# Kernel tuning notes

Hardware: AMD Instinct MI355X
Metric: run time of the kernel (lower is better)

Reference implementation:

```python
import jax, jax.numpy as jnp
import numpy as np

N_HEADS = 8
FACTOR = 5


def layer_norm(x, g, b, eps=1e-5):
    m = x.mean(-1, keepdims=True)
    v = ((x - m) ** 2).mean(-1, keepdims=True)
    return (x - m) / jnp.sqrt(v + eps) * g + b


def prob_attn(q, k, v, factor, key):
    # q,k,v: [B,H,L,E]; mask_flag=False path of ProbAttention
    B, H, L, E = q.shape
    U = min(int(factor * np.ceil(np.log(L))), L)  # sample_k == n_top (L_Q == L_K)
    idx = jax.random.randint(key, (L, U), 0, L)   # random KV sample per query pos
    k_samp = k[:, :, idx, :]                      # gather: [B,H,L,U,E]
    qk_samp = jnp.einsum('bhle,bhlue->bhlu', q, k_samp)
    M = qk_samp.max(-1) - qk_samp.sum(-1) / L     # sparsity measure [B,H,L]
    _, top = jax.lax.top_k(M, U)                  # top-u query indices [B,H,U]
    q_red = jnp.take_along_axis(q, top[..., None], axis=2)  # [B,H,U,E]
    scores = jnp.einsum('bhue,bhke->bhuk', q_red, k) * (1.0 / np.sqrt(E))
    attn = jax.nn.softmax(scores, axis=-1)
    upd = jnp.einsum('bhuk,bhkd->bhud', attn, v)  # [B,H,U,D]
    ctx = jnp.broadcast_to(v.mean(axis=2, keepdims=True), (B, H, L, v.shape[-1]))
    bi = jnp.arange(B)[:, None, None]
    hi = jnp.arange(H)[None, :, None]
    return ctx.at[bi, hi, top].set(upd)          # scatter reduced context


def informer_fwd(x_enc, x_mark_enc, conv_w, Wq, bq, Wk, bk, Wv, bv, Wo, bo,
                 W1, b1, W2, b2, g1, be1, g2, be2, gF, bF, fc_w, fc_b):
    B, L, C = x_enc.shape
    D = conv_w.shape[0]
    H = N_HEADS
    dh = D // H
    # TokenEmbedding: circular Conv1d k=3, no bias
    xp = jnp.transpose(x_enc, (0, 2, 1))                      # [B,C,L]
    xp = jnp.concatenate([xp[..., -1:], xp, xp[..., :1]], axis=-1)
    tok = jax.lax.conv_general_dilated(xp, conv_w, (1,), 'VALID',
                                       dimension_numbers=('NCH', 'OIH', 'NCH'))
    tok = jnp.transpose(tok, (0, 2, 1))                       # [B,L,D]
    # PositionalEmbedding (sinusoid)
    pos = jnp.arange(L, dtype=jnp.float32)[:, None]
    div = jnp.exp(jnp.arange(0, D, 2, dtype=jnp.float32) * (-np.log(10000.0) / D))
    pe = jnp.zeros((L, D), jnp.float32)
    pe = pe.at[:, 0::2].set(jnp.sin(pos * div)).at[:, 1::2].set(jnp.cos(pos * div))
    x = tok + pe
    n_layers = Wq.shape[0]
    for l in range(n_layers):
        q = (x @ Wq[l].T + bq[l]).reshape(B, L, H, dh).transpose(0, 2, 1, 3)
        k = (x @ Wk[l].T + bk[l]).reshape(B, L, H, dh).transpose(0, 2, 1, 3)
        v = (x @ Wv[l].T + bv[l]).reshape(B, L, H, dh).transpose(0, 2, 1, 3)
        ctx = prob_attn(q, k, v, FACTOR, jax.random.fold_in(jax.random.key(42), l))
        # NOTE: original code does .view(B, L, -1) on [B,H,L,dh] WITHOUT transposing
        out = ctx.reshape(B, L, H * dh)
        x = x + (out @ Wo[l].T + bo[l])
        x = layer_norm(x, g1[l], be1[l])
        y = jax.nn.relu(x @ W1[l].T + b1[l]) @ W2[l].T + b2[l]   # 1x1 convs == dense
        x = layer_norm(x + y, g2[l], be2[l])
    x = layer_norm(x, gF, bF)
    out = x * x_mark_enc[..., None]
    out = out.reshape(B, -1)
    return out @ fc_w.T + fc_b


def setup_inputs() -> dict:
    B, L, C, D, H, Dff, EL, NC = 8, 1024, 32, 512, 8, 2048, 3, 16
    key = jax.random.key(0)
    ks = jax.random.split(key, 16)
    rn = lambda k, s, sc=0.02: sc * jax.random.normal(k, s, dtype=jnp.float32)
    return {
        'x_enc': jax.random.normal(ks[0], (B, L, C), dtype=jnp.float32),
        'x_mark_enc': jax.random.uniform(ks[1], (B, L), dtype=jnp.float32),
        'conv_w': rn(ks[2], (D, C, 3), 0.1),
        'Wq': rn(ks[3], (EL, D, D)), 'bq': jnp.zeros((EL, D)),
        'Wk': rn(ks[4], (EL, D, D)), 'bk': jnp.zeros((EL, D)),
        'Wv': rn(ks[5], (EL, D, D)), 'bv': jnp.zeros((EL, D)),
        'Wo': rn(ks[6], (EL, D, D)), 'bo': jnp.zeros((EL, D)),
        'W1': rn(ks[7], (EL, Dff, D)), 'b1': jnp.zeros((EL, Dff)),
        'W2': rn(ks[8], (EL, D, Dff)), 'b2': jnp.zeros((EL, D)),
        'g1': jnp.ones((EL, D)), 'be1': jnp.zeros((EL, D)),
        'g2': jnp.ones((EL, D)), 'be2': jnp.zeros((EL, D)),
        'gF': jnp.ones((D,)), 'bF': jnp.zeros((D,)),
        'fc_w': rn(ks[9], (NC, L * D)), 'fc_b': jnp.zeros((NC,)),
    }


def reference(x_enc, x_mark_enc, conv_w, Wq, bq, Wk, bk, Wv, bv, Wo, bo,
              W1, b1, W2, b2, g1, be1, g2, be2, gF, bF, fc_w, fc_b):
    return informer_fwd(x_enc, x_mark_enc, conv_w, Wq, bq, Wk, bk, Wv, bv, Wo, bo,
                        W1, b1, W2, b2, g1, be1, g2, be2, gF, bF, fc_w, fc_b)
```

## Files before the change

kernel.cpp:

```cpp
#include <hip/hip_runtime.h>
#include <stdint.h>
#include <math.h>

#define LSEQ   1024
#define DMODEL 512
#define NH     8
#define DH     64
#define DFF    2048
#define NB     8
#define NLAYER 3
#define UTOP   35
#define NCLS   16
#define WPERL  3145728

typedef unsigned short u16;
typedef _Float16 f16x8 __attribute__((ext_vector_type(8)));
typedef __attribute__((ext_vector_type(4))) float f32x4;

__device__ __forceinline__ u16 f2h(float f) {
  _Float16 h = (_Float16)f;
  return __builtin_bit_cast(u16, h);
}
__device__ __forceinline__ float h2f(u16 b) {
  return (float)__builtin_bit_cast(_Float16, b);
}

#define GLDS16(gsrc, ldst)                                                        \
  __builtin_amdgcn_global_load_lds(                                              \
      (const __attribute__((address_space(1))) void*)(gsrc),                     \
      (__attribute__((address_space(3))) void*)(ldst), 16, 0, 0)

__host__ __device__ __forceinline__ uint32_t rotl32(uint32_t x, int d) {
  return (x << d) | (x >> (32 - d));
}
__host__ __device__ inline void tf2x32(uint32_t k0, uint32_t k1,
                                       uint32_t c0, uint32_t c1,
                                       uint32_t& o0, uint32_t& o1) {
  uint32_t ks2 = k0 ^ k1 ^ 0x1BD11BDAu;
  uint32_t x0 = c0 + k0, x1 = c1 + k1;
#define TF_R4(a,b,c,d) \
  x0 += x1; x1 = rotl32(x1,(a)); x1 ^= x0; \
  x0 += x1; x1 = rotl32(x1,(b)); x1 ^= x0; \
  x0 += x1; x1 = rotl32(x1,(c)); x1 ^= x0; \
  x0 += x1; x1 = rotl32(x1,(d)); x1 ^= x0;
  TF_R4(13,15,26,6)   x0 += k1;  x1 += ks2 + 1u;
  TF_R4(17,29,16,24)  x0 += ks2; x1 += k0 + 2u;
  TF_R4(13,15,26,6)   x0 += k0;  x1 += k1 + 3u;
  TF_R4(17,29,16,24)  x0 += k1;  x1 += ks2 + 4u;
  TF_R4(13,15,26,6)   x0 += ks2; x1 += k0 + 5u;
#undef TF_R4
  o0 = x0; o1 = x1;
}

__global__ void __launch_bounds__(256) gen_idx_kernel(uint32_t k0, uint32_t k1,
                                                      int* idx) {
  int i = blockIdx.x * 256 + threadIdx.x;
  if (i >= LSEQ * UTOP) return;
  uint32_t a, b;
  tf2x32(k0, k1, 0u, (uint32_t)i, a, b);
  idx[i] = (int)((a ^ b) & (LSEQ - 1));
}

__global__ void __launch_bounds__(256) cvt_all(
    const float* __restrict__ Wq, const float* __restrict__ Wk,
    const float* __restrict__ Wv, const float* __restrict__ Wo,
    const float* __restrict__ W1, const float* __restrict__ W2,
    u16* __restrict__ dst) {
  const size_t total = (size_t)NLAYER * WPERL;
  for (size_t i4 = ((size_t)blockIdx.x * 256 + threadIdx.x) * 4;
       i4 < total; i4 += (size_t)gridDim.x * 256 * 4) {
    int l = (int)(i4 / WPERL);
    int off = (int)(i4 % WPERL);
    const float* src; size_t so;
    if (off < 262144)       { src = Wq; so = (size_t)l * 262144  + off; }
    else if (off < 524288)  { src = Wk; so = (size_t)l * 262144  + off - 262144; }
    else if (off < 786432)  { src = Wv; so = (size_t)l * 262144  + off - 524288; }
    else if (off < 1048576) { src = Wo; so = (size_t)l * 262144  + off - 786432; }
    else if (off < 2097152) { src = W1; so = (size_t)l * 1048576 + off - 1048576; }
    else                    { src = W2; so = (size_t)l * 1048576 + off - 2097152; }
    float4 v = *(const float4*)&src[so];
    ushort4 h;
    h.x = f2h(v.x); h.y = f2h(v.y); h.z = f2h(v.z); h.w = f2h(v.w);
    *(ushort4*)&dst[i4] = h;
  }
}

__global__ void __launch_bounds__(256) conv_pe(const float* __restrict__ xe,
                                               const float* __restrict__ w,
                                               float* __restrict__ xout,
                                               u16* __restrict__ xh) {
  const int d0 = blockIdx.x * 64;
  const int l0 = blockIdx.y * 32;
  const int b  = blockIdx.z;
  const int tid = threadIdx.x;
  const int dl = tid & 63;
  const int lq = tid >> 6;
  __shared__ float ws_[64][97];
  __shared__ float xs[32][37];

  for (int i = tid; i < 64 * 96; i += 256) {
    int dd = i / 96, cc = i - dd * 96;
    ws_[dd][cc] = w[(size_t)(d0 + dd) * 96 + cc];
  }
  for (int i = tid; i < 34 * 32; i += 256) {
    int r = i >> 5, c = i & 31;
    int row = (l0 - 1 + r + LSEQ) & (LSEQ - 1);
    xs[c][r] = xe[((size_t)b * LSEQ + row) * 32 + c];
  }

  const int d = d0 + dl;
  float div = expf((float)(d & ~1) * (-9.210340371976184f / 512.0f));
  float pe[8];
  #pragma unroll
  for (int j = 0; j < 8; ++j) {
    float arg = (float)(l0 + lq * 8 + j) * div;
    pe[j] = (d & 1) ? cosf(arg) : sinf(arg);
  }
  __syncthreads();

  float acc[8] = {};
  #pragma unroll 4
  for (int c = 0; c < 32; ++c) {
    float w0 = ws_[dl][c * 3 + 0];
    float w1 = ws_[dl][c * 3 + 1];
    float w2 = ws_[dl][c * 3 + 2];
    float xv[10];
    #pragma unroll
    for (int r = 0; r < 10; ++r) xv[r] = xs[c][lq * 8 + r];
    #pragma unroll
    for (int j = 0; j < 8; ++j)
      acc[j] += xv[j] * w0 + xv[j + 1] * w1 + xv[j + 2] * w2;
  }
  #pragma unroll
  for (int j = 0; j < 8; ++j) {
    int l = l0 + lq * 8 + j;
    float v = acc[j] + pe[j];
    size_t m = (size_t)b * LSEQ + l;
    xout[m * DMODEL + d] = v;
    xh[m * DMODEL + d] = f2h(v);
  }
}

__global__ void __launch_bounds__(512, 2) gemm256(
    const u16* __restrict__ A, const u16* __restrict__ W,
    const float* __restrict__ bias, const float* __restrict__ bias_k,
    const float* __restrict__ bias_v,
    float* __restrict__ Cf, u16* __restrict__ C2,
    int Kseg, int N, int mode) {
  __shared__ u16 As[2][256 * 64];
  __shared__ u16 Bs[2][256 * 64];
  const int tid = threadIdx.x;
  const int lane = tid & 63, wv = tid >> 6;
  const int wm = wv >> 2, wn = wv & 3;
  const int m0 = blockIdx.y * 256, n0 = blockIdx.x * 256;
  const int lrow = lane >> 3;
  const int kgS = (lane & 7) ^ lrow;
  const int nt = Kseg >> 6;

  f32x4 acc[8][4];
  #pragma unroll
  for (int i = 0; i < 8; ++i)
    #pragma unroll
    for (int j = 0; j < 4; ++j) acc[i][j] = (f32x4){0.f, 0.f, 0.f, 0.f};

  auto STAGE = [&](int kv, int buf) {
    #pragma unroll
    for (int r = 0; r < 4; ++r) {
      int seg = wv * 4 + r;
      int row = seg * 8 + lrow;
      GLDS16(A + (size_t)(m0 + row) * Kseg + kv + kgS * 8, &As[buf][seg * 512]);
      GLDS16(W + (size_t)(n0 + row) * Kseg + kv + kgS * 8, &Bs[buf][seg * 512]);
    }
  };

  STAGE(0, 0);
  asm volatile("s_waitcnt vmcnt(0)" ::: "memory");
  __builtin_amdgcn_s_barrier();
  for (int t = 0; t < nt; ++t) {
    const int cur = t & 1;
    if (t + 1 < nt) STAGE((t + 1) * 64, cur ^ 1);
    #pragma unroll
    for (int kk = 0; kk < 2; ++kk) {
      int kg = kk * 4 + (lane >> 4);
      f16x8 af[8], bf[4];
      #pragma unroll
      for (int mi = 0; mi < 8; ++mi) {
        int row = wm * 128 + mi * 16 + (lane & 15);
        af[mi] = *(const f16x8*)&As[cur][row * 64 + ((kg ^ (row & 7)) << 3)];
      }
      #pragma unroll
      for (int ni = 0; ni < 4; ++ni) {
        int row = wn * 64 + ni * 16 + (lane & 15);
        bf[ni] = *(const f16x8*)&Bs[cur][row * 64 + ((kg ^ (row & 7)) << 3)];
      }
      #pragma unroll
      for (int mi = 0; mi < 8; ++mi)
        #pragma unroll
        for (int ni = 0; ni < 4; ++ni)
          acc[mi][ni] = __builtin_amdgcn_mfma_f32_16x16x32_f16(
              af[mi], bf[ni], acc[mi][ni], 0, 0, 0);
    }
    asm volatile("s_waitcnt vmcnt(0) lgkmcnt(0)" ::: "memory");
    __builtin_amdgcn_s_barrier();
  }

  const int colb = n0 + wn * 64 + (lane & 15);
  const int rowb = m0 + wm * 128 + ((lane >> 4) << 2);
  #pragma unroll
  for (int mi = 0; mi < 8; ++mi) {
    #pragma unroll
    for (int ni = 0; ni < 4; ++ni) {
      int gcol = colb + ni * 16;
      float bv;
      if (mode == 3) {
        int mat = gcol >> 9, c = gcol & 511;
        bv = (mat == 0 ? bias : (mat == 1 ? bias_k : bias_v))[c];
      } else {
        bv = bias[gcol];
      }
      #pragma unroll
      for (int j = 0; j < 4; ++j) {
        int grow = rowb + mi * 16 + j;
        float v = acc[mi][ni][j] + bv;
        if (mode == 1) {
          C2[(size_t)grow * N + gcol] = f2h(fmaxf(v, 0.f));
        } else {
          int mat = gcol >> 9, c = gcol & 511;
          Cf[(size_t)mat * (NB * LSEQ * DMODEL) +
             (size_t)(grow >> 10) * (NH * LSEQ * DH) +
             (size_t)(c >> 6) * (LSEQ * DH) +
             (size_t)(grow & (LSEQ - 1)) * DH + (c & (DH - 1))] = v;
        }
      }
    }
  }
}

__global__ void __launch_bounds__(256) gemm_cat(
    const u16* __restrict__ A, const u16* __restrict__ W,
    const float* __restrict__ bias, const float* __restrict__ resid,
    float* __restrict__ Cf, float* __restrict__ Cf1,
    int Kseg, int kslice, int N) {
  __shared__ u16 As[2][128 * 64];
  __shared__ u16 Bs[2][128 * 64];
  const int tid = threadIdx.x;
  const int lane = tid & 63, wv = tid >> 6;
  const int wm = wv >> 1, wn = wv & 1;
  const int m0 = blockIdx.y * 128, n0 = blockIdx.x * 128;
  const int lrow = lane >> 3;
  const int kgS = (lane & 7) ^ lrow;
  const int kv0 = blockIdx.z * kslice;
  const int nt = kslice >> 6;

  f32x4 acc[4][4];
  #pragma unroll
  for (int i = 0; i < 4; ++i)
    #pragma unroll
    for (int j = 0; j < 4; ++j) acc[i][j] = (f32x4){0.f, 0.f, 0.f, 0.f};

  auto STAGE = [&](int kv, int buf) {
    #pragma unroll
    for (int r = 0; r < 4; ++r) {
      int seg = wv * 4 + r;
      int row = seg * 8 + lrow;
      GLDS16(A + (size_t)(m0 + row) * Kseg + kv + kgS * 8, &As[buf][seg * 512]);
      GLDS16(W + (size_t)(n0 + row) * Kseg + kv + kgS * 8, &Bs[buf][seg * 512]);
    }
  };

  STAGE(kv0, 0);
  asm volatile("s_waitcnt vmcnt(0)" ::: "memory");
  __builtin_amdgcn_s_barrier();
  for (int t = 0; t < nt; ++t) {
    const int cur = t & 1;
    if (t + 1 < nt) STAGE(kv0 + (t + 1) * 64, cur ^ 1);
    #pragma unroll
    for (int kk = 0; kk < 2; ++kk) {
      int kg = kk * 4 + (lane >> 4);
      f16x8 af[4], bf[4];
      #pragma unroll
      for (int mi = 0; mi < 4; ++mi) {
        int row = wm * 64 + mi * 16 + (lane & 15);
        af[mi] = *(const f16x8*)&As[cur][row * 64 + ((kg ^ (row & 7)) << 3)];
      }
      #pragma unroll
      for (int ni = 0; ni < 4; ++ni) {
        int row = wn * 64 + ni * 16 + (lane & 15);
        bf[ni] = *(const f16x8*)&Bs[cur][row * 64 + ((kg ^ (row & 7)) << 3)];
      }
      #pragma unroll
      for (int mi = 0; mi < 4; ++mi)
        #pragma unroll
        for (int ni = 0; ni < 4; ++ni)
          acc[mi][ni] = __builtin_amdgcn_mfma_f32_16x16x32_f16(
              af[mi], bf[ni], acc[mi][ni], 0, 0, 0);
    }
    asm volatile("s_waitcnt vmcnt(0) lgkmcnt(0)" ::: "memory");
    __builtin_amdgcn_s_barrier();
  }

  const int colb = n0 + wn * 64 + (lane & 15);
  const int rowb = m0 + wm * 64 + ((lane >> 4) << 2);
  const bool z0 = (blockIdx.z == 0);
  float* co = z0 ? Cf : Cf1;
  #pragma unroll
  for (int mi = 0; mi < 4; ++mi) {
    #pragma unroll
    for (int ni = 0; ni < 4; ++ni) {
      int gcol = colb + ni * 16;
      float bv = z0 ? bias[gcol] : 0.f;
      #pragma unroll
      for (int j = 0; j < 4; ++j) {
        int grow = rowb + mi * 16 + j;
        float v = acc[mi][ni][j] + bv;
        size_t o = (size_t)grow * N + gcol;
        if (z0 && resid) v += resid[o];
        co[o] = v;
      }
    }
  }
}

__global__ void __launch_bounds__(256) sampled_m(const float* __restrict__ q,
                                                 const float* __restrict__ k,
                                                 const int* __restrict__ idx,
                                                 float* __restrict__ M) {
  const int g = threadIdx.x >> 6, t = threadIdx.x & 63;
  const int bid = blockIdx.x;
  const int c6 = bid & 63;
  const int bh = ((c6 & 7) << 3) | (c6 >> 3);
  const int l = (bid >> 6) * 4 + g;
  const int bhl = (bh << 10) | l;
  const float4 qv = *(const float4*)&q[(size_t)bhl * DH + (t & 15) * 4];
  const float* kbase = k + (((size_t)bh) << 10) * DH;
  const int* ip = idx + l * UTOP;
  float vmax = -INFINITY, vsum = 0.f;
  #pragma unroll
  for (int b = 0; b < 9; ++b) {
    int u = b * 4 + (t >> 4);
    bool valid = (u < UTOP);
    int kr = valid ? ip[u] : 0;
    float4 kv = *(const float4*)&kbase[(size_t)kr * DH + (t & 15) * 4];
    float p = qv.x * kv.x + qv.y * kv.y + qv.z * kv.z + qv.w * kv.w;
    p += __shfl_xor(p, 1);
    p += __shfl_xor(p, 2);
    p += __shfl_xor(p, 4);
    p += __shfl_xor(p, 8);
    if (valid) { vmax = fmaxf(vmax, p); vsum += p; }
  }
  vmax = fmaxf(vmax, __shfl_down(vmax, 32));
  vmax = fmaxf(vmax, __shfl_down(vmax, 16));
  vsum += __shfl_down(vsum, 32);
  vsum += __shfl_down(vsum, 16);
  if (t == 0) M[bhl] = vmax - vsum * (1.0f / (float)LSEQ);
}

__global__ void __launch_bounds__(256) topk35(const float* __restrict__ M,
                                              int* __restrict__ top) {
  int bh = blockIdx.x;
  int t = threadIdx.x;
  __shared__ float mv[LSEQ];
  __shared__ float rv[256];
  __shared__ int   ri[256];
  for (int i = t; i < LSEQ; i += 256) mv[i] = M[(size_t)bh * LSEQ + i];
  __syncthreads();
  for (int it = 0; it < UTOP; ++it) {
    float bestv = -INFINITY; int besti = 0x7fffffff;
    for (int i = t; i < LSEQ; i += 256) {
      float v = mv[i];
      if (v > bestv || (v == bestv && i < besti)) { bestv = v; besti = i; }
    }
    rv[t] = bestv; ri[t] = besti;
    __syncthreads();
    for (int s = 128; s; s >>= 1) {
      if (t < s) {
        float v2 = rv[t + s]; int i2 = ri[t + s];
        if (v2 > rv[t] || (v2 == rv[t] && i2 < ri[t])) { rv[t] = v2; ri[t] = i2; }
      }
      __syncthreads();
    }
    if (t == 0) { top[bh * UTOP + it] = ri[0]; mv[ri[0]] = -INFINITY; }
    __syncthreads();
  }
}

__global__ void __launch_bounds__(256) vmean_k(const float* __restrict__ v,
                                               float* __restrict__ vm) {
  int bh = blockIdx.x, t = threadIdx.x;
  int e = t & 63, c = t >> 6;
  float s = 0.f;
  for (int l = c * 256; l < (c + 1) * 256; ++l)
    s += v[((size_t)bh * LSEQ + l) * DH + e];
  __shared__ float pr[4][64];
  pr[c][e] = s; __syncthreads();
  if (t < 64)
    vm[bh * DH + t] = (pr[0][t] + pr[1][t] + pr[2][t] + pr[3][t]) * (1.0f / (float)LSEQ);
}

__global__ void __launch_bounds__(256) ctx_fillb(const float* __restrict__ vm,
                                                 u16* __restrict__ ctxh) {
  int j4 = (blockIdx.x * 256 + threadIdx.x) * 4;
  int bh = j4 >> 16;
  int e = j4 & 63;
  float4 v = *(const float4*)&vm[bh * DH + e];
  ushort4 h;
  h.x = f2h(v.x); h.y = f2h(v.y); h.z = f2h(v.z); h.w = f2h(v.w);
  *(ushort4*)&ctxh[(size_t)(j4 >> 9) * 512 + (j4 & 511)] = h;
}

__global__ void __launch_bounds__(256) attn_rows(const float* __restrict__ q,
                                                 const float* __restrict__ k,
                                                 const float* __restrict__ v,
                                                 const int* __restrict__ top,
                                                 u16* __restrict__ ctxh) {
  const int bid = blockIdx.x;
  const int c6 = bid & 63, uc = bid >> 6;
  const int bh = ((c6 & 7) << 3) | (c6 >> 3);
  const int t = threadIdx.x;
  const int lane = t & 63, wvi = t >> 6;
  __shared__ float qs[5][DH];
  __shared__ float sc[5][LSEQ];
  __shared__ float red[32];
  __shared__ float part[4][5][DH];
  __shared__ float mxs[5], invs[5];
  int rows[5];
  #pragma unroll
  for (int i = 0; i < 5; ++i) rows[i] = top[bh * UTOP + uc * 5 + i];
  for (int i = t; i < 5 * DH; i += 256) {
    int u = i >> 6, e = i & 63;
    qs[u][e] = q[((size_t)bh * LSEQ + rows[u]) * DH + e];
  }
  __syncthreads();

  float mloc[5] = {-INFINITY, -INFINITY, -INFINITY, -INFINITY, -INFINITY};
  for (int kk = t; kk < LSEQ; kk += 256) {
    float4 kr[16];
    const float4* kp = (const float4*)&k[((size_t)bh * LSEQ + kk) * DH];
    #pragma unroll
    for (int e = 0; e < 16; ++e) kr[e] = kp[e];
    #pragma unroll
    for (int u = 0; u < 5; ++u) {
      const float4* q4 = (const float4*)qs[u];
      float d = 0.f;
      #pragma unroll
      for (int e = 0; e < 16; ++e) {
        float4 qv = q4[e];
        d += qv.x * kr[e].x + qv.y * kr[e].y + qv.z * kr[e].z + qv.w * kr[e].w;
      }
      d *= 0.125f;
      sc[u][kk] = d;
      mloc[u] = fmaxf(mloc[u], d);
    }
  }
  #pragma unroll
  for (int u = 0; u < 5; ++u) {
    float m = mloc[u];
    #pragma unroll
    for (int off = 32; off; off >>= 1) m = fmaxf(m, __shfl_down(m, off));
    if (lane == 0) red[u * 4 + wvi] = m;
  }
  __syncthreads();
  if (t < 5)
    mxs[t] = fmaxf(fmaxf(red[t * 4], red[t * 4 + 1]),
                   fmaxf(red[t * 4 + 2], red[t * 4 + 3]));
  __syncthreads();

  float sloc[5] = {};
  for (int kk = t; kk < LSEQ; kk += 256) {
    #pragma unroll
    for (int u = 0; u < 5; ++u) {
      float p = expf(sc[u][kk] - mxs[u]);
      sc[u][kk] = p;
      sloc[u] += p;
    }
  }
  #pragma unroll
  for (int u = 0; u < 5; ++u) {
    float s = sloc[u];
    #pragma unroll
    for (int off = 32; off; off >>= 1) s += __shfl_down(s, off);
    if (lane == 0) red[u * 4 + wvi] = s;
  }
  __syncthreads();
  if (t < 5)
    invs[t] = 1.0f / (red[t * 4] + red[t * 4 + 1] + red[t * 4 + 2] + red[t * 4 + 3]);
  __syncthreads();

  int e = t & 63, cq = t >> 6;
  float acc[5] = {};
  for (int kk = cq * 256; kk < (cq + 1) * 256; ++kk) {
    float vv = v[((size_t)bh * LSEQ + kk) * DH + e];
    #pragma unroll
    for (int u = 0; u < 5; ++u) acc[u] += sc[u][kk] * vv;
  }
  #pragma unroll
  for (int u = 0; u < 5; ++u) part[cq][u][e] = acc[u];
  __syncthreads();
  for (int i = t; i < 5 * DH; i += 256) {
    int u = i >> 6, ee = i & 63;
    float s = (part[0][u][ee] + part[1][u][ee] + part[2][u][ee] + part[3][u][ee]) * invs[u];
    size_t lin = ((size_t)bh * LSEQ + rows[u]) * DH + ee;
    ctxh[(lin >> 9) * 512 + (lin & 511)] = f2h(s);
  }
}

__global__ void __launch_bounds__(256) ln_k(const float* __restrict__ in,
                                            const float* __restrict__ in2,
                                            const float* __restrict__ g,
                                            const float* __restrict__ be,
                                            float* __restrict__ out,
                                            u16* __restrict__ oh,
                                            const float* __restrict__ mark) {
  int row = blockIdx.x, t = threadIdx.x;
  size_t o0 = (size_t)row * DMODEL + t, o1 = o0 + 256;
  float x0 = in[o0], x1 = in[o1];
  if (in2) { x0 += in2[o0]; x1 += in2[o1]; }
  __shared__ float red[256];
  red[t] = x0 + x1; __syncthreads();
  for (int s = 128; s; s >>= 1) { if (t < s) red[t] += red[t + s]; __syncthreads(); }
  float mean = red[0] * (1.0f / DMODEL);
  __syncthreads();
  float d0 = x0 - mean, d1 = x1 - mean;
  red[t] = d0 * d0 + d1 * d1; __syncthreads();
  for (int s = 128; s; s >>= 1) { if (t < s) red[t] += red[t + s]; __syncthreads(); }
  float rstd = 1.0f / sqrtf(red[0] * (1.0f / DMODEL) + 1e-5f);
  float v0 = d0 * rstd * g[t] + be[t];
  float v1 = d1 * rstd * g[t + 256] + be[t + 256];
  if (mark) { float mk = mark[row]; v0 *= mk; v1 *= mk; }
  if (out) { out[o0] = v0; out[o1] = v1; }
  if (oh) {
    oh[o0] = f2h(v0);
    oh[o1] = f2h(v1);
  }
}

__global__ void __launch_bounds__(256) fc_stage1(const float* __restrict__ y,
                                                 const float* __restrict__ fw,
                                                 float* __restrict__ part) {
  int blk = blockIdx.x;
  int k0 = blk * 1024;
  int tid = threadIdx.x;
  __shared__ float ys[NB][1024];
  #pragma unroll
  for (int b = 0; b < NB; ++b)
    *(float4*)&ys[b][tid * 4] = *(const float4*)&y[(size_t)b * (LSEQ * DMODEL) + k0 + tid * 4];
  __syncthreads();
  int c = tid & 15, ks = tid >> 4;
  float acc[NB] = {};
  const float* wp = fw + (size_t)c * (LSEQ * DMODEL) + k0 + ks * 64;
  for (int j = 0; j < 16; ++j) {
    int jj = (j + ks) & 15;
    float4 w4 = *(const float4*)&wp[jj * 4];
    #pragma unroll
    for (int b = 0; b < NB; ++b) {
      float4 yv = *(const float4*)&ys[b][ks * 64 + jj * 4];
      acc[b] += yv.x * w4.x + yv.y * w4.y + yv.z * w4.z + yv.w * w4.w;
    }
  }
  __shared__ float rs[16][128];
  #pragma unroll
  for (int b = 0; b < NB; ++b) rs[ks][b * 16 + c] = acc[b];
  __syncthreads();
  if (tid < 128) {
    float s = 0.f;
    #pragma unroll
    for (int i = 0; i < 16; ++i) s += rs[i][tid];
    part[(size_t)tid * 512 + blk] = s;
  }
}

__global__ void __launch_bounds__(128) fc_stage2(const float* __restrict__ part,
                                                 const float* __restrict__ fb,
                                                 float* __restrict__ out) {
  int bc = threadIdx.x;
  float s = 0.f;
  for (int i = 0; i < 512; ++i) s += part[(size_t)bc * 512 + i];
  out[bc] = s + fb[bc & 15];
}

extern "C" void kernel_launch(void* const* d_in, const int* in_sizes, int n_in,
                              void* d_out, int out_size, void* d_ws, size_t ws_size,
                              hipStream_t stream) {
  (void)in_sizes; (void)n_in; (void)out_size; (void)ws_size;
  const float* x_enc  = (const float*)d_in[0];
  const float* x_mark = (const float*)d_in[1];
  const float* conv_w = (const float*)d_in[2];
  const float* Wq = (const float*)d_in[3];
  const float* bq = (const float*)d_in[4];
  const float* Wk = (const float*)d_in[5];
  const float* bk = (const float*)d_in[6];
  const float* Wv = (const float*)d_in[7];
  const float* bv = (const float*)d_in[8];
  const float* Wo = (const float*)d_in[9];
  const float* bo = (const float*)d_in[10];
  const float* W1 = (const float*)d_in[11];
  const float* b1 = (const float*)d_in[12];
  const float* W2 = (const float*)d_in[13];
  const float* b2 = (const float*)d_in[14];
  const float* g1 = (const float*)d_in[15];
  const float* be1= (const float*)d_in[16];
  const float* g2 = (const float*)d_in[17];
  const float* be2= (const float*)d_in[18];
  const float* gF = (const float*)d_in[19];
  const float* bF = (const float*)d_in[20];
  const float* fcw= (const float*)d_in[21];
  const float* fcb= (const float*)d_in[22];
  float* out = (float*)d_out;

  const size_t NBLD = (size_t)NB * LSEQ * DMODEL;
  float* ws   = (float*)d_ws;
  float* xb   = ws;
  float* pre0 = xb   + NBLD;
  float* qb   = pre0 + NBLD;
  float* kb   = qb   + NBLD;
  float* vb   = kb   + NBLD;
  u16*  xh    = (u16*)(vb + NBLD);
  u16*  ctxh  = xh + NBLD;
  u16*  Wcat  = ctxh + NBLD;
  float* Mb   = (float*)(Wcat + (size_t)NLAYER * WPERL);
  float* vm   = Mb + (size_t)NB * NH * LSEQ;
  float* part = vm + NB * NH * DH;
  int* idxb   = (int*)(part + 512 * 128);
  int* topb   = idxb + LSEQ * UTOP;
  u16* hidh   = (u16*)qb;
  float* preB = qb;
  float* preC = vb;

  cvt_all<<<2048, 256, 0, stream>>>(Wq, Wk, Wv, Wo, W1, W2, Wcat);

  {
    dim3 gc(8, 32, NB);
    conv_pe<<<gc, 256, 0, stream>>>(x_enc, conv_w, xb, xh);
  }

  dim3 gqkv(6,  32);
  dim3 gw1 (8,  32);
  dim3 gwo (4,  64, 2);
  dim3 gw2 (4,  64, 2);

  for (int l = 0; l < NLAYER; ++l) {
    const u16* Wl    = Wcat + (size_t)l * WPERL;
    const u16* Wc_qkv= Wl;
    const u16* Wc_o  = Wl + 786432;
    const u16* Wc_1  = Wl + 1048576;
    const u16* Wc_2  = Wl + 2097152;

    gemm256<<<gqkv, 512, 0, stream>>>(xh, Wc_qkv,
                                      bq + l*DMODEL, bk + l*DMODEL, bv + l*DMODEL,
                                      qb, nullptr, 512, 1536, 3);

    uint32_t lk0, lk1, k2_0, k2_1;
    tf2x32(0u, 42u, 0u, (uint32_t)l, lk0, lk1);
    tf2x32(lk0, lk1, 0u, 1u, k2_0, k2_1);
    gen_idx_kernel<<<140, 256, 0, stream>>>(k2_0, k2_1, idxb);
    sampled_m<<<NB * NH * LSEQ / 4, 256, 0, stream>>>(qb, kb, idxb, Mb);
    topk35<<<NB * NH, 256, 0, stream>>>(Mb, topb);
    vmean_k<<<NB * NH, 256, 0, stream>>>(vb, vm);
    ctx_fillb<<<(NB * NH * LSEQ * DH) / 1024, 256, 0, stream>>>(vm, ctxh);
    attn_rows<<<448, 256, 0, stream>>>(qb, kb, vb, topb, ctxh);

    gemm_cat<<<gwo, 256, 0, stream>>>(ctxh, Wc_o, bo + l*DMODEL,
                                      xb, pre0, preB, 512, 256, 512);
    ln_k<<<NB * LSEQ, 256, 0, stream>>>(pre0, preB, g1 + l*DMODEL, be1 + l*DMODEL,
                                        xb, xh, nullptr);

    gemm256<<<gw1, 512, 0, stream>>>(xh, Wc_1,
                                     b1 + l*DFF, nullptr, nullptr,
                                     nullptr, hidh, 512, 2048, 1);
    gemm_cat<<<gw2, 256, 0, stream>>>(hidh, Wc_2, b2 + l*DMODEL,
                                      xb, pre0, preC, 2048, 1024, 512);
    ln_k<<<NB * LSEQ, 256, 0, stream>>>(pre0, preC, g2 + l*DMODEL, be2 + l*DMODEL,
                                        xb, xh, nullptr);
  }

  ln_k<<<NB * LSEQ, 256, 0, stream>>>(xb, nullptr, gF, bF, pre0, nullptr, x_mark);
  fc_stage1<<<512, 256, 0, stream>>>(pre0, fcw, part);
  fc_stage2<<<1, 128, 0, stream>>>(part, fcb, out);
}
```

Before: 986.9 us.

## Overlap GEMM tile loads with one barrier, swizzle blocks, widen attn_rows

Both GEMM kernels now wait only for the older tile's loads (vmcnt(8)) after issuing the next prefetch, and keep one barrier before compute instead of a full drain at the end of each iteration. They also remap block IDs with an 8-way swizzle, meant to improve L2 reuse across neighbouring blocks. Separately, attn_rows moves to 512 threads with chunked key loads to cut register pressure and add parallelism. The reduced barrier scheme risks a race if the vmcnt count does not match the actual outstanding loads. The swizzle assumes the block count divides by 8.

```diff
diff --git a/kernel.cpp b/kernel.cpp
--- a/kernel.cpp
+++ b/kernel.cpp
@@ -152,7 +152,10 @@
   const int tid = threadIdx.x;
   const int lane = tid & 63, wv = tid >> 6;
   const int wm = wv >> 2, wn = wv & 3;
-  const int m0 = blockIdx.y * 256, n0 = blockIdx.x * 256;
+  const int pid = blockIdx.y * gridDim.x + blockIdx.x;
+  const int cpx = (gridDim.x * gridDim.y) >> 3;
+  const int swz = (pid & 7) * cpx + (pid >> 3);
+  const int m0 = (swz / gridDim.x) * 256, n0 = (swz % gridDim.x) * 256;
   const int lrow = lane >> 3;
   const int kgS = (lane & 7) ^ lrow;
   const int nt = Kseg >> 6;
@@ -174,11 +177,16 @@
   };
 
   STAGE(0, 0);
-  asm volatile("s_waitcnt vmcnt(0)" ::: "memory");
-  __builtin_amdgcn_s_barrier();
   for (int t = 0; t < nt; ++t) {
     const int cur = t & 1;
-    if (t + 1 < nt) STAGE((t + 1) * 64, cur ^ 1);
+    if (t + 1 < nt) {
+      STAGE((t + 1) * 64, cur ^ 1);
+      asm volatile("s_waitcnt vmcnt(8)" ::: "memory");
+    } else {
+      asm volatile("s_waitcnt vmcnt(0)" ::: "memory");
+    }
+    __builtin_amdgcn_s_barrier();
+    __builtin_amdgcn_sched_barrier(0);
     #pragma unroll
     for (int kk = 0; kk < 2; ++kk) {
       int kg = kk * 4 + (lane >> 4);
@@ -200,7 +208,6 @@
           acc[mi][ni] = __builtin_amdgcn_mfma_f32_16x16x32_f16(
               af[mi], bf[ni], acc[mi][ni], 0, 0, 0);
     }
-    asm volatile("s_waitcnt vmcnt(0) lgkmcnt(0)" ::: "memory");
     __builtin_amdgcn_s_barrier();
   }
 
@@ -246,7 +253,10 @@
   const int tid = threadIdx.x;
   const int lane = tid & 63, wv = tid >> 6;
   const int wm = wv >> 1, wn = wv & 1;
-  const int m0 = blockIdx.y * 128, n0 = blockIdx.x * 128;
+  const int pid = blockIdx.y * gridDim.x + blockIdx.x;
+  const int cpx = (gridDim.x * gridDim.y) >> 3;
+  const int swz = (pid & 7) * cpx + (pid >> 3);
+  const int m0 = (swz / gridDim.x) * 128, n0 = (swz % gridDim.x) * 128;
   const int lrow = lane >> 3;
   const int kgS = (lane & 7) ^ lrow;
   const int kv0 = blockIdx.z * kslice;
@@ -269,11 +279,16 @@
   };
 
   STAGE(kv0, 0);
-  asm volatile("s_waitcnt vmcnt(0)" ::: "memory");
-  __builtin_amdgcn_s_barrier();
   for (int t = 0; t < nt; ++t) {
     const int cur = t & 1;
-    if (t + 1 < nt) STAGE(kv0 + (t + 1) * 64, cur ^ 1);
+    if (t + 1 < nt) {
+      STAGE(kv0 + (t + 1) * 64, cur ^ 1);
+      asm volatile("s_waitcnt vmcnt(8)" ::: "memory");
+    } else {
+      asm volatile("s_waitcnt vmcnt(0)" ::: "memory");
+    }
+    __builtin_amdgcn_s_barrier();
+    __builtin_amdgcn_sched_barrier(0);
     #pragma unroll
     for (int kk = 0; kk < 2; ++kk) {
       int kg = kk * 4 + (lane >> 4);
@@ -295,7 +310,6 @@
           acc[mi][ni] = __builtin_amdgcn_mfma_f32_16x16x32_f16(
               af[mi], bf[ni], acc[mi][ni], 0, 0, 0);
     }
-    asm volatile("s_waitcnt vmcnt(0) lgkmcnt(0)" ::: "memory");
     __builtin_amdgcn_s_barrier();
   }
 
@@ -408,7 +422,7 @@
   *(ushort4*)&ctxh[(size_t)(j4 >> 9) * 512 + (j4 & 511)] = h;
 }
 
-__global__ void __launch_bounds__(256) attn_rows(const float* __restrict__ q,
+__global__ void __launch_bounds__(512) attn_rows(const float* __restrict__ q,
                                                  const float* __restrict__ k,
                                                  const float* __restrict__ v,
                                                  const int* __restrict__ top,
@@ -420,36 +434,44 @@
   const int lane = t & 63, wvi = t >> 6;
   __shared__ float qs[5][DH];
   __shared__ float sc[5][LSEQ];
-  __shared__ float red[32];
-  __shared__ float part[4][5][DH];
+  __shared__ float red[5][8];
+  __shared__ float part[8][5][DH];
   __shared__ float mxs[5], invs[5];
   int rows[5];
   #pragma unroll
   for (int i = 0; i < 5; ++i) rows[i] = top[bh * UTOP + uc * 5 + i];
-  for (int i = t; i < 5 * DH; i += 256) {
+  for (int i = t; i < 5 * DH; i += 512) {
     int u = i >> 6, e = i & 63;
     qs[u][e] = q[((size_t)bh * LSEQ + rows[u]) * DH + e];
   }
   __syncthreads();
 
   float mloc[5] = {-INFINITY, -INFINITY, -INFINITY, -INFINITY, -INFINITY};
-  for (int kk = t; kk < LSEQ; kk += 256) {
-    float4 kr[16];
+  #pragma unroll
+  for (int it = 0; it < 2; ++it) {
+    int kk = t + it * 512;
     const float4* kp = (const float4*)&k[((size_t)bh * LSEQ + kk) * DH];
-    #pragma unroll
-    for (int e = 0; e < 16; ++e) kr[e] = kp[e];
+    float d[5] = {};
+    #pragma unroll
+    for (int c0 = 0; c0 < 16; c0 += 8) {
+      float4 kr[8];
+      #pragma unroll
+      for (int e = 0; e < 8; ++e) kr[e] = kp[c0 + e];
+      #pragma unroll
+      for (int u = 0; u < 5; ++u) {
+        const float4* q4 = (const float4*)qs[u];
+        #pragma unroll
+        for (int e = 0; e < 8; ++e) {
+          float4 qv = q4[c0 + e];
+          d[u] += qv.x * kr[e].x + qv.y * kr[e].y + qv.z * kr[e].z + qv.w * kr[e].w;
+        }
+      }
+    }
     #pragma unroll
     for (int u = 0; u < 5; ++u) {
-      const float4* q4 = (const float4*)qs[u];
-      float d = 0.f;
-      #pragma unroll
-      for (int e = 0; e < 16; ++e) {
-        float4 qv = q4[e];
-        d += qv.x * kr[e].x + qv.y * kr[e].y + qv.z * kr[e].z + qv.w * kr[e].w;
-      }
-      d *= 0.125f;
-      sc[u][kk] = d;
-      mloc[u] = fmaxf(mloc[u], d);
+      float dv = d[u] * 0.125f;
+      sc[u][kk] = dv;
+      mloc[u] = fmaxf(mloc[u], dv);
     }
   }
   #pragma unroll
@@ -457,16 +479,21 @@
     float m = mloc[u];
     #pragma unroll
     for (int off = 32; off; off >>= 1) m = fmaxf(m, __shfl_down(m, off));
-    if (lane == 0) red[u * 4 + wvi] = m;
-  }
-  __syncthreads();
-  if (t < 5)
-    mxs[t] = fmaxf(fmaxf(red[t * 4], red[t * 4 + 1]),
-                   fmaxf(red[t * 4 + 2], red[t * 4 + 3]));
+    if (lane == 0) red[u][wvi] = m;
+  }
+  __syncthreads();
+  if (t < 5) {
+    float m = red[t][0];
+    #pragma unroll
+    for (int i = 1; i < 8; ++i) m = fmaxf(m, red[t][i]);
+    mxs[t] = m;
+  }
   __syncthreads();
 
   float sloc[5] = {};
-  for (int kk = t; kk < LSEQ; kk += 256) {
+  #pragma unroll
+  for (int it = 0; it < 2; ++it) {
+    int kk = t + it * 512;
     #pragma unroll
     for (int u = 0; u < 5; ++u) {
       float p = expf(sc[u][kk] - mxs[u]);
@@ -479,16 +506,20 @@
     float s = sloc[u];
     #pragma unroll
     for (int off = 32; off; off >>= 1) s += __shfl_down(s, off);
-    if (lane == 0) red[u * 4 + wvi] = s;
-  }
-  __syncthreads();
-  if (t < 5)
-    invs[t] = 1.0f / (red[t * 4] + red[t * 4 + 1] + red[t * 4 + 2] + red[t * 4 + 3]);
+    if (lane == 0) red[u][wvi] = s;
+  }
+  __syncthreads();
+  if (t < 5) {
+    float s = 0.f;
+    #pragma unroll
+    for (int i = 0; i < 8; ++i) s += red[t][i];
+    invs[t] = 1.0f / s;
+  }
   __syncthreads();
 
   int e = t & 63, cq = t >> 6;
   float acc[5] = {};
-  for (int kk = cq * 256; kk < (cq + 1) * 256; ++kk) {
+  for (int kk = cq * 128; kk < (cq + 1) * 128; ++kk) {
     float vv = v[((size_t)bh * LSEQ + kk) * DH + e];
     #pragma unroll
     for (int u = 0; u < 5; ++u) acc[u] += sc[u][kk] * vv;
@@ -496,9 +527,12 @@
   #pragma unroll
   for (int u = 0; u < 5; ++u) part[cq][u][e] = acc[u];
   __syncthreads();
-  for (int i = t; i < 5 * DH; i += 256) {
+  for (int i = t; i < 5 * DH; i += 512) {
     int u = i >> 6, ee = i & 63;
-    float s = (part[0][u][ee] + part[1][u][ee] + part[2][u][ee] + part[3][u][ee]) * invs[u];
+    float s = 0.f;
+    #pragma unroll
+    for (int c = 0; c < 8; ++c) s += part[c][u][ee];
+    s *= invs[u];
     size_t lin = ((size_t)bh * LSEQ + rows[u]) * DH + ee;
     ctxh[(lin >> 9) * 512 + (lin & 511)] = f2h(s);
   }
@@ -657,7 +691,7 @@
     topk35<<<NB * NH, 256, 0, stream>>>(Mb, topb);
     vmean_k<<<NB * NH, 256, 0, stream>>>(vb, vm);
     ctx_fillb<<<(NB * NH * LSEQ * DH) / 1024, 256, 0, stream>>>(vm, ctxh);
-    attn_rows<<<448, 256, 0, stream>>>(qb, kb, vb, topb, ctxh);
+    attn_rows<<<448, 512, 0, stream>>>(qb, kb, vb, topb, ctxh);
 
     gemm_cat<<<gwo, 256, 0, stream>>>(ctxh, Wc_o, bo + l*DMODEL,
                                       xb, pre0, preB, 512, 256, 512);
```

New measurement: 998.3 us. No clear change (+1.2%).
